# Kernel optimization log

Hardware: AMD Instinct MI355X
Metric: run time of the kernel (lower is better)

The kernel has to match this reference:

```python
import jax, jax.numpy as jnp
import numpy as np

B, A, F = 8192, 8, 256      # batch, n_agents, per-agent obs feature dim
NA = 16                     # n_actions per agent
H1, H2 = 1024, 1024
OBS_D = A * F               # 2048 flattened obs dim
ACT_D = A * NA              # 128 joint action dim
IN_D = OBS_D + ACT_D        # 2176 MLP input dim


def setup_inputs() -> dict:
    key = jax.random.key(0)
    ks = jax.random.split(key, 8)
    s = 0.02
    return {
        "obs": jax.random.normal(ks[0], (B, A, F), dtype=jnp.float32),
        "all_actions": jax.random.uniform(ks[1], (B, ACT_D), dtype=jnp.float32),
        # per-agent stacked MLP params (agent axis first)
        "W1": jax.random.normal(ks[2], (A, IN_D, H1), dtype=jnp.float32) * s,
        "b1": jnp.zeros((A, H1), dtype=jnp.float32),
        "W2": jax.random.normal(ks[3], (A, H1, H2), dtype=jnp.float32) * s,
        "b2": jnp.zeros((A, H2), dtype=jnp.float32),
        "W3": jax.random.normal(ks[4], (A, H2, NA), dtype=jnp.float32) * s,
        "b3": jnp.zeros((A, NA), dtype=jnp.float32),
    }


def reference(obs, all_actions, W1, b1, W2, b2, W3, b3):
    b_s = obs.shape[0]
    obs_flat = obs.reshape(b_s, OBS_D)                      # [B, A*F]
    # mask[a, g] = 0 on agent a's own action block, 1 elsewhere
    mask = 1.0 - jnp.repeat(jnp.eye(A, dtype=obs.dtype), NA, axis=1)  # [A, A*NA]
    # split W1 into obs / action columns (equivalent to concat-then-dense)
    W1o = W1[:, :OBS_D, :]                                  # [A, OBS_D, H1]
    W1a = W1[:, OBS_D:, :]                                  # [A, ACT_D, H1]
    h1 = jax.nn.relu(
        jnp.einsum("bd,adh->bah", obs_flat, W1o)
        + jnp.einsum("bg,ag,agh->bah", all_actions, mask, W1a)
        + b1
    )                                                        # [B, A, H1]
    h2 = jax.nn.relu(jnp.einsum("bah,ahk->bak", h1, W2) + b2)  # [B, A, H2]
    out = jnp.einsum("bak,akn->ban", h2, W3) + b3              # [B, A, NA]
    return out.reshape(b_s, A * NA)
```

## Files before the change

kernel.cpp:

```cpp
#include <hip/hip_runtime.h>
#include <hip/hip_bf16.h>
#include <cstdint>
#include <cstddef>

typedef __bf16 bf16;
typedef __attribute__((ext_vector_type(8))) __bf16 bf16x8;
typedef __attribute__((ext_vector_type(4))) float f32x4;
typedef __attribute__((ext_vector_type(4))) int i32x4;
typedef __attribute__((address_space(3))) const bf16* lds_cp;

#define B_SZ  8192
#define NAGENT 8
#define NA_N  16
#define OBS_DD 2048
#define ACT_DD 128
#define IN_DD 2176
#define H1_D  1024
#define H2_D  1024

#define BM 256
#define BN 256
#define BK 64
#define GRID_M (B_SZ / BM)
#define GRID_N (1024 / BN)

__device__ __forceinline__ void gload16(const void* g, void* l) {
    __builtin_amdgcn_global_load_lds(
        (__attribute__((address_space(1))) void*)(g),
        (__attribute__((address_space(3))) void*)(l), 16, 0, 0);
}

__global__ void k_prep(const float* __restrict__ obs, const float* __restrict__ act,
                       bf16* __restrict__ xb, const float* __restrict__ b3,
                       float* __restrict__ out, const float* __restrict__ W3,
                       bf16* __restrict__ w3t) {
    const int NX = B_SZ * (IN_DD / 8);
    const int NO = B_SZ * 128 / 4;
    const int NW3 = NAGENT * NA_N * H2_D;
    int idx = blockIdx.x * blockDim.x + threadIdx.x;
    if (idx < NX) {
        const int chunks = IN_DD / 8;
        int b = idx / chunks;
        int c8 = idx - b * chunks;
        const float* src = (c8 < OBS_DD / 8)
            ? (obs + (size_t)b * OBS_DD + c8 * 8)
            : (act + (size_t)b * ACT_DD + (c8 - OBS_DD / 8) * 8);
        float4 v0 = ((const float4*)src)[0];
        float4 v1 = ((const float4*)src)[1];
        bf16x8 o;
        o[0] = (bf16)v0.x; o[1] = (bf16)v0.y; o[2] = (bf16)v0.z; o[3] = (bf16)v0.w;
        o[4] = (bf16)v1.x; o[5] = (bf16)v1.y; o[6] = (bf16)v1.z; o[7] = (bf16)v1.w;
        ((bf16x8*)(xb + (size_t)b * IN_DD))[c8] = o;
    } else if (idx < NX + NO) {
        int i = idx - NX;
        int c = (i & 31) * 4;
        float4 v = make_float4(b3[c], b3[c + 1], b3[c + 2], b3[c + 3]);
        ((float4*)out)[i] = v;
    } else if (idx < NX + NO + NW3) {
        int i = idx - NX - NO;
        int a = i / (NA_N * H2_D);
        int n = (i / H2_D) % NA_N;
        int k = i % H2_D;
        w3t[i] = (bf16)W3[(size_t)a * H2_D * NA_N + (size_t)k * NA_N + n];
    }
}

__global__ void k_transpose_w12(const float* __restrict__ W1, bf16* __restrict__ W1T,
                                const float* __restrict__ W2, bf16* __restrict__ W2T) {
    __shared__ float tile[32][33];
    const int z = blockIdx.z;
    const bool isW1 = (z < 8);
    const int a = isW1 ? z : z - 8;
    const int K = isW1 ? IN_DD : H1_D;
    const int H = 1024;
    const int maskStart = isW1 ? OBS_DD : (1 << 30);
    if (!isW1 && blockIdx.x >= (H1_D / 32)) return;
    const float* s = (isW1 ? W1 : W2) + (size_t)a * K * H;
    bf16* d = (isW1 ? W1T : W2T) + (size_t)a * K * H;
    int k0 = blockIdx.x * 32, h0 = blockIdx.y * 32;
    int tx = threadIdx.x, ty = threadIdx.y;
    #pragma unroll
    for (int i = 0; i < 32; i += 8) {
        int k = k0 + ty + i;
        float v = s[(size_t)k * H + h0 + tx];
        if (k >= maskStart) {
            int g = k - maskStart;
            if ((g >> 4) == a) v = 0.f;
        }
        tile[ty + i][tx] = v;
    }
    __syncthreads();
    #pragma unroll
    for (int i = 0; i < 32; i += 8) {
        d[(size_t)(h0 + ty + i) * K + k0 + tx] = (bf16)tile[tx][ty + i];
    }
}

#define DSR4(d0, d1, d2, d3, addr, O0, O1, O2, O3)                      \
    asm volatile("ds_read_b128 %0, %4 offset:" #O0 "\n\t"               \
                 "ds_read_b128 %1, %4 offset:" #O1 "\n\t"               \
                 "ds_read_b128 %2, %4 offset:" #O2 "\n\t"               \
                 "ds_read_b128 %3, %4 offset:" #O3                      \
                 : "=&v"(d0), "=&v"(d1), "=&v"(d2), "=&v"(d3)           \
                 : "v"(addr))
#define DSR2(d0, d1, addr, O0, O1)                                      \
    asm volatile("ds_read_b128 %0, %2 offset:" #O0 "\n\t"               \
                 "ds_read_b128 %1, %2 offset:" #O1                      \
                 : "=&v"(d0), "=&v"(d1) : "v"(addr))

#define BC(x) __builtin_bit_cast(bf16x8, x)

template<int FUSE>
__global__ __launch_bounds__(512, 1)
void k_gemm256(const bf16* __restrict__ Ain, size_t aStride, int lda,
               const bf16* __restrict__ Bw, const float* __restrict__ bias,
               bf16* __restrict__ Cout, size_t cStride, int K,
               int aOff, int gridZ,
               const bf16* __restrict__ W3Tp, float* __restrict__ outp) {
    extern __shared__ bf16 lds[];

    const int tid = threadIdx.x;
    const int w = tid >> 6;
    const int l = tid & 63;

    int flat = blockIdx.x + GRID_M * (blockIdx.y + GRID_N * blockIdx.z);
    int q8 = (GRID_M * GRID_N * gridZ) >> 3;
    int lin2 = (flat & 7) * q8 + (flat >> 3);
    const int ntile = lin2 % GRID_N;
    int rest = lin2 / GRID_N;
    const int mt = rest % GRID_M;
    const int az = rest / GRID_M;
    const int aw = az + aOff;

    const int rowBase = mt * BM;
    const int colBase = ntile * BN;
    const bf16* Aag = Ain + (size_t)az * aStride;
    const bf16* Bag = Bw + (size_t)aw * (size_t)1024 * K;

    const int wr = (w >> 2) * 128;
    const int wc = (w & 3) * 64;
    const int lr = l & 15;
    const int lq = l >> 4;

    const int rowA = (wr + lr) * BK;
    const int rowB = (wc + lr) * BK;
    const int ck0 = ((lq ^ (lr & 7)) * 8);
    const int ck1 = (((4 + lq) ^ (lr & 7)) * 8);

    const int sRow = w * 16 + (l >> 3);
    const int sCol = ((l & 7) ^ (l >> 3)) * 8;
    const bf16* pA0 = Aag + (size_t)(rowBase + sRow) * lda + sCol;
    const bf16* pA1 = Aag + (size_t)(rowBase + 128 + sRow) * lda + sCol;
    const bf16* pB0 = Bag + (size_t)(colBase + sRow) * K + sCol;
    const bf16* pB1 = Bag + (size_t)(colBase + 128 + sRow) * K + sCol;
    const size_t l8a = (size_t)8 * lda;
    const size_t l8b = (size_t)8 * K;

    const int nkt = K / BK;

#define STAGE_A(t1, half) do {                                              \
        const bf16* g_ = ((half) ? pA1 : pA0) + (t1) * BK;                  \
        bf16* d_ = &lds[(((t1) & 1) * 16384) + (half) * 8192 + w * 1024];   \
        gload16(g_, d_);                                                    \
        gload16(g_ + l8a, d_ + 512);                                        \
    } while (0)
#define STAGE_B(t2, half) do {                                              \
        const bf16* g_ = ((half) ? pB1 : pB0) + (t2) * BK;                  \
        bf16* d_ = &lds[32768 + (((t2) & 1) * 16384) + (half) * 8192 + w * 1024]; \
        gload16(g_, d_);                                                    \
        gload16(g_ + l8b, d_ + 512);                                        \
    } while (0)

    f32x4 acc[8][4] = {};
    i32x4 rb0, rb1, rb2, rb3, rb4, rb5, rb6, rb7;
    i32x4 a0, a1, a2, a3, a4, a5, a6, a7, z0, z1;

#define CL8(M0, A0r, A1r, Bx0, Bx1, Bx2, Bx3)                               \
    do {                                                                    \
        acc[M0+0][0] = __builtin_amdgcn_mfma_f32_16x16x32_bf16(BC(A0r), BC(Bx0), acc[M0+0][0], 0, 0, 0); \
        acc[M0+1][0] = __builtin_amdgcn_mfma_f32_16x16x32_bf16(BC(A1r), BC(Bx0), acc[M0+1][0], 0, 0, 0); \
        acc[M0+0][1] = __builtin_amdgcn_mfma_f32_16x16x32_bf16(BC(A0r), BC(Bx1), acc[M0+0][1], 0, 0, 0); \
        acc[M0+1][1] = __builtin_amdgcn_mfma_f32_16x16x32_bf16(BC(A1r), BC(Bx1), acc[M0+1][1], 0, 0, 0); \
        acc[M0+0][2] = __builtin_amdgcn_mfma_f32_16x16x32_bf16(BC(A0r), BC(Bx2), acc[M0+0][2], 0, 0, 0); \
        acc[M0+1][2] = __builtin_amdgcn_mfma_f32_16x16x32_bf16(BC(A1r), BC(Bx2), acc[M0+1][2], 0, 0, 0); \
        acc[M0+0][3] = __builtin_amdgcn_mfma_f32_16x16x32_bf16(BC(A0r), BC(Bx3), acc[M0+0][3], 0, 0, 0); \
        acc[M0+1][3] = __builtin_amdgcn_mfma_f32_16x16x32_bf16(BC(A1r), BC(Bx3), acc[M0+1][3], 0, 0, 0); \
    } while (0)

#define WAITL(N)                                                            \
    asm volatile("s_waitcnt lgkmcnt(" #N ")" ::: "memory");                 \
    __builtin_amdgcn_sched_barrier(0)

    STAGE_A(0, 0); STAGE_A(0, 1);
    STAGE_B(0, 0); STAGE_B(0, 1);
    asm volatile("s_waitcnt vmcnt(0)" ::: "memory");
    __builtin_amdgcn_s_barrier();

    for (int t = 0; t < nkt; ++t) {
        const int dbuf = (t & 1) * 16384;
        lds_cp adrA0 = (lds_cp)lds + (dbuf + rowA + ck0);
        lds_cp adrA1 = (lds_cp)lds + (dbuf + rowA + ck1);
        lds_cp adrB0 = (lds_cp)lds + (32768 + dbuf + rowB + ck0);
        lds_cp adrB1 = (lds_cp)lds + (32768 + dbuf + rowB + ck1);

        DSR2(a0, a1, adrA0, 0, 2048);
        DSR4(rb0, rb1, rb2, rb3, adrB0, 0, 2048, 4096, 6144);
        DSR2(a2, a3, adrA0, 4096, 6144);

        WAITL(2);
        __builtin_amdgcn_s_setprio(1);
        CL8(0, a0, a1, rb0, rb1, rb2, rb3);
        __builtin_amdgcn_s_setprio(0);

        DSR2(a4, a5, adrA0, 8192, 10240);
        WAITL(2);
        __builtin_amdgcn_s_setprio(1);
        CL8(2, a2, a3, rb0, rb1, rb2, rb3);
        __builtin_amdgcn_s_setprio(0);

        DSR2(a6, a7, adrA0, 12288, 14336);
        if (t + 1 < nkt) {
            STAGE_A(t + 1, 0); STAGE_A(t + 1, 1);
            STAGE_B(t + 1, 0); STAGE_B(t + 1, 1);
        }
        WAITL(2);
        __builtin_amdgcn_s_setprio(1);
        CL8(4, a4, a5, rb0, rb1, rb2, rb3);
        __builtin_amdgcn_s_setprio(0);

        DSR2(z0, z1, adrA1, 0, 2048);
        DSR4(rb4, rb5, rb6, rb7, adrB1, 0, 2048, 4096, 6144);
        WAITL(6);
        __builtin_amdgcn_s_setprio(1);
        CL8(6, a6, a7, rb0, rb1, rb2, rb3);
        __builtin_amdgcn_s_setprio(0);

        DSR2(a0, a1, adrA1, 4096, 6144);
        WAITL(2);
        __builtin_amdgcn_s_setprio(1);
        CL8(0, z0, z1, rb4, rb5, rb6, rb7);
        __builtin_amdgcn_s_setprio(0);

        DSR2(a2, a3, adrA1, 8192, 10240);
        WAITL(2);
        __builtin_amdgcn_s_setprio(1);
        CL8(2, a0, a1, rb4, rb5, rb6, rb7);
        __builtin_amdgcn_s_setprio(0);

        DSR2(a4, a5, adrA1, 12288, 14336);
        WAITL(2);
        __builtin_amdgcn_s_setprio(1);
        CL8(4, a2, a3, rb4, rb5, rb6, rb7);
        __builtin_amdgcn_s_setprio(0);

        asm volatile("s_waitcnt vmcnt(0)" ::: "memory");
        WAITL(0);
        __builtin_amdgcn_s_setprio(1);
        CL8(6, a4, a5, rb4, rb5, rb6, rb7);
        __builtin_amdgcn_s_setprio(0);

        __builtin_amdgcn_s_barrier();
    }
#undef STAGE_A
#undef STAGE_B
#undef CL8
#undef WAITL

    __syncthreads();
    const float* bAg = bias + (size_t)aw * 1024;
    float bb4[4];
    #pragma unroll
    for (int n = 0; n < 4; ++n) bb4[n] = bAg[colBase + wc + n * 16 + lr];
    #pragma unroll
    for (int m = 0; m < 8; ++m)
        #pragma unroll
        for (int n = 0; n < 4; ++n)
            #pragma unroll
            for (int r = 0; r < 4; ++r) {
                float v = acc[m][n][r] + bb4[n];
                v = fmaxf(v, 0.f);
                int row = wr + m * 16 + lq * 4 + r;
                int col = wc + n * 16 + lr;
                lds[row * 256 + ((((col >> 3) ^ (row & 7)) << 3) | (col & 7))] = (bf16)v;
            }
    __syncthreads();

    if constexpr (!FUSE) {
        bf16* Cg = Cout + (size_t)az * cStride + (size_t)rowBase * 1024 + colBase;
        const int er = tid >> 5;
        const int ec = tid & 31;
        #pragma unroll
        for (int i = 0; i < 16; ++i) {
            int row = i * 16 + er;
            int phys = ec ^ (row & 7);
            *(bf16x8*)&Cg[(size_t)row * 1024 + ec * 8] =
                *(const bf16x8*)&lds[row * 256 + phys * 8];
        }
    } else {
        const bf16* w3a = W3Tp + (size_t)aw * NA_N * H2_D;
        f32x4 oacc[2] = {};
        const int frow0 = w * 32;
        #pragma unroll
        for (int ks = 0; ks < 8; ++ks) {
            bf16x8 bfrag = *(const bf16x8*)&w3a[(size_t)lr * H2_D + colBase + ks * 32 + lq * 8];
            #pragma unroll
            for (int mm = 0; mm < 2; ++mm) {
                int row = frow0 + mm * 16 + lr;
                int lc = (ks * 4 + lq) ^ (row & 7);
                bf16x8 afrag = *(const bf16x8*)&lds[row * 256 + lc * 8];
                oacc[mm] = __builtin_amdgcn_mfma_f32_16x16x32_bf16(afrag, bfrag, oacc[mm], 0, 0, 0);
            }
        }
        #pragma unroll
        for (int mm = 0; mm < 2; ++mm)
            #pragma unroll
            for (int r = 0; r < 4; ++r)
                atomicAdd(&outp[(size_t)(rowBase + frow0 + mm * 16 + lq * 4 + r) * 128
                                + aw * NA_N + lr], oacc[mm][r]);
    }
}

extern "C" void kernel_launch(void* const* d_in, const int* in_sizes, int n_in,
                              void* d_out, int out_size, void* d_ws, size_t ws_size,
                              hipStream_t stream) {
    const float* obs = (const float*)d_in[0];
    const float* act = (const float*)d_in[1];
    const float* W1 = (const float*)d_in[2];
    const float* b1 = (const float*)d_in[3];
    const float* W2 = (const float*)d_in[4];
    const float* b2 = (const float*)d_in[5];
    const float* W3 = (const float*)d_in[6];
    const float* b3 = (const float*)d_in[7];
    float* out = (float*)d_out;

    const size_t SZ_XB  = (size_t)B_SZ * IN_DD * 2;
    const size_t SZ_W1T = (size_t)NAGENT * H1_D * IN_DD * 2;
    const size_t SZ_W2T = (size_t)NAGENT * H1_D * H2_D * 2;
    const size_t SZ_W3T = (size_t)NAGENT * NA_N * H2_D * 2;
    const size_t SZ_H1  = (size_t)B_SZ * H1_D * 2;
    const size_t SZ_FIX = SZ_XB + SZ_W1T + SZ_W2T + SZ_W3T;

    char* ws = (char*)d_ws;
    bf16* Xb  = (bf16*)ws;
    bf16* W1T = (bf16*)(ws + SZ_XB);
    bf16* W2T = (bf16*)(ws + SZ_XB + SZ_W1T);
    bf16* W3T = (bf16*)(ws + SZ_XB + SZ_W1T + SZ_W2T);
    char* hbase = ws + SZ_FIX;

    int G = 8;
    while (G > 1 && ws_size < SZ_FIX + (size_t)G * SZ_H1) G >>= 1;

    (void)hipFuncSetAttribute((const void*)k_gemm256<0>,
                              hipFuncAttributeMaxDynamicSharedMemorySize, 131072);
    (void)hipFuncSetAttribute((const void*)k_gemm256<1>,
                              hipFuncAttributeMaxDynamicSharedMemorySize, 131072);

    {
        const int NX = B_SZ * (IN_DD / 8);
        const int NO = B_SZ * 128 / 4;
        const int NW3 = NAGENT * NA_N * H2_D;
        int n = NX + NO + NW3;
        k_prep<<<(n + 255) / 256, 256, 0, stream>>>(obs, act, Xb, b3, out, W3, W3T);
    }
    k_transpose_w12<<<dim3(IN_DD / 32, 1024 / 32, 16), dim3(32, 8), 0, stream>>>(
        W1, W1T, W2, W2T);

    const size_t agElems = (size_t)B_SZ * H1_D;
    bf16* h1 = (bf16*)hbase;

    for (int g0 = 0; g0 < NAGENT; g0 += G) {
        k_gemm256<0><<<dim3(GRID_M, GRID_N, G), 512, 131072, stream>>>(
            Xb, 0, IN_DD, W1T, b1, h1, agElems, IN_DD, g0, G, nullptr, nullptr);
        k_gemm256<1><<<dim3(GRID_M, GRID_N, G), 512, 131072, stream>>>(
            h1, agElems, H1_D, W2T, b2, nullptr, 0, H1_D, g0, G, W3T, out);
    }
    (void)in_sizes; (void)n_in; (void)out_size;
}
```

Before: 407.1 us.

## Switch main GEMM to 32x32x16 MFMA with new LDS swizzle and read schedule

Replaces the 16x16x32 bf16 MFMA tiling in the 256x256 GEMM with 32x32x16 MFMA instructions, using 4x2 accumulators of 16 floats per wave instead of 8x4 of 4. The LDS staging swizzle gains an extra XOR term, and the fragment reads are reorganised into four k-slices with ping-pong register sets. The aim is fewer LDS fragment reads per FLOP and higher MFMA throughput per instruction. The epilogue row/column mapping is rewritten for the 32x32 output layout. This risks bank conflicts and a swizzle mismatch with the store pattern, and the prefetch now issues earlier in the iteration.

```diff
diff --git a/kernel.cpp b/kernel.cpp
--- a/kernel.cpp
+++ b/kernel.cpp
@@ -6,6 +6,7 @@
 typedef __bf16 bf16;
 typedef __attribute__((ext_vector_type(8))) __bf16 bf16x8;
 typedef __attribute__((ext_vector_type(4))) float f32x4;
+typedef __attribute__((ext_vector_type(16))) float f32x16;
 typedef __attribute__((ext_vector_type(4))) int i32x4;
 typedef __attribute__((address_space(3))) const bf16* lds_cp;
 
@@ -29,6 +30,9 @@
         (__attribute__((address_space(1))) void*)(g),
         (__attribute__((address_space(3))) void*)(l), 16, 0, 0);
 }
+
+#define MFMA32(a, b, c) __builtin_amdgcn_mfma_f32_32x32x16_bf16((a), (b), (c), 0, 0, 0)
+#define BC(x) __builtin_bit_cast(bf16x8, x)
 
 __global__ void k_prep(const float* __restrict__ obs, const float* __restrict__ act,
                        bf16* __restrict__ xb, const float* __restrict__ b3,
@@ -108,8 +112,6 @@
                  "ds_read_b128 %1, %2 offset:" #O1                      \
                  : "=&v"(d0), "=&v"(d1) : "v"(addr))
 
-#define BC(x) __builtin_bit_cast(bf16x8, x)
-
 template<int FUSE>
 __global__ __launch_bounds__(512, 1)
 void k_gemm256(const bf16* __restrict__ Ain, size_t aStride, int lda,
@@ -139,16 +141,22 @@
 
     const int wr = (w >> 2) * 128;
     const int wc = (w & 3) * 64;
+    const int r31 = l & 31;
+    const int hi = l >> 5;
+    const int x7 = l & 7;
+    const int hb = (l >> 4) & 1;
     const int lr = l & 15;
     const int lq = l >> 4;
 
-    const int rowA = (wr + lr) * BK;
-    const int rowB = (wc + lr) * BK;
-    const int ck0 = ((lq ^ (lr & 7)) * 8);
-    const int ck1 = (((4 + lq) ^ (lr & 7)) * 8);
+    const int arow = (wr + r31) * BK;
+    const int brow = (wc + r31) * BK;
+    const int cs0 = ((0 + hi) ^ x7 ^ (hb << 2)) * 8;
+    const int cs1 = ((2 + hi) ^ x7 ^ (hb << 2)) * 8;
+    const int cs2 = ((4 + hi) ^ x7 ^ (hb << 2)) * 8;
+    const int cs3 = ((6 + hi) ^ x7 ^ (hb << 2)) * 8;
 
     const int sRow = w * 16 + (l >> 3);
-    const int sCol = ((l & 7) ^ (l >> 3)) * 8;
+    const int sCol = ((l & 7) ^ (l >> 3) ^ ((w & 1) << 2)) * 8;
     const bf16* pA0 = Aag + (size_t)(rowBase + sRow) * lda + sCol;
     const bf16* pA1 = Aag + (size_t)(rowBase + 128 + sRow) * lda + sCol;
     const bf16* pB0 = Bag + (size_t)(colBase + sRow) * K + sCol;
@@ -171,20 +179,20 @@
         gload16(g_ + l8b, d_ + 512);                                        \
     } while (0)
 
-    f32x4 acc[8][4] = {};
-    i32x4 rb0, rb1, rb2, rb3, rb4, rb5, rb6, rb7;
-    i32x4 a0, a1, a2, a3, a4, a5, a6, a7, z0, z1;
-
-#define CL8(M0, A0r, A1r, Bx0, Bx1, Bx2, Bx3)                               \
+    f32x16 acc[4][2] = {};
+    i32x4 fa0, fa1, fa2, fa3, fb0, fb1;
+    i32x4 ga0, ga1, ga2, ga3, gb0, gb1;
+
+#define CLK(A0r, A1r, A2r, A3r, B0r, B1r)                                   \
     do {                                                                    \
-        acc[M0+0][0] = __builtin_amdgcn_mfma_f32_16x16x32_bf16(BC(A0r), BC(Bx0), acc[M0+0][0], 0, 0, 0); \
-        acc[M0+1][0] = __builtin_amdgcn_mfma_f32_16x16x32_bf16(BC(A1r), BC(Bx0), acc[M0+1][0], 0, 0, 0); \
-        acc[M0+0][1] = __builtin_amdgcn_mfma_f32_16x16x32_bf16(BC(A0r), BC(Bx1), acc[M0+0][1], 0, 0, 0); \
-        acc[M0+1][1] = __builtin_amdgcn_mfma_f32_16x16x32_bf16(BC(A1r), BC(Bx1), acc[M0+1][1], 0, 0, 0); \
-        acc[M0+0][2] = __builtin_amdgcn_mfma_f32_16x16x32_bf16(BC(A0r), BC(Bx2), acc[M0+0][2], 0, 0, 0); \
-        acc[M0+1][2] = __builtin_amdgcn_mfma_f32_16x16x32_bf16(BC(A1r), BC(Bx2), acc[M0+1][2], 0, 0, 0); \
-        acc[M0+0][3] = __builtin_amdgcn_mfma_f32_16x16x32_bf16(BC(A0r), BC(Bx3), acc[M0+0][3], 0, 0, 0); \
-        acc[M0+1][3] = __builtin_amdgcn_mfma_f32_16x16x32_bf16(BC(A1r), BC(Bx3), acc[M0+1][3], 0, 0, 0); \
+        acc[0][0] = MFMA32(BC(A0r), BC(B0r), acc[0][0]);                    \
+        acc[1][0] = MFMA32(BC(A1r), BC(B0r), acc[1][0]);                    \
+        acc[0][1] = MFMA32(BC(A0r), BC(B1r), acc[0][1]);                    \
+        acc[1][1] = MFMA32(BC(A1r), BC(B1r), acc[1][1]);                    \
+        acc[2][0] = MFMA32(BC(A2r), BC(B0r), acc[2][0]);                    \
+        acc[3][0] = MFMA32(BC(A3r), BC(B0r), acc[3][0]);                    \
+        acc[2][1] = MFMA32(BC(A2r), BC(B1r), acc[2][1]);                    \
+        acc[3][1] = MFMA32(BC(A3r), BC(B1r), acc[3][1]);                    \
     } while (0)
 
 #define WAITL(N)                                                            \
@@ -198,89 +206,72 @@
 
     for (int t = 0; t < nkt; ++t) {
         const int dbuf = (t & 1) * 16384;
-        lds_cp adrA0 = (lds_cp)lds + (dbuf + rowA + ck0);
-        lds_cp adrA1 = (lds_cp)lds + (dbuf + rowA + ck1);
-        lds_cp adrB0 = (lds_cp)lds + (32768 + dbuf + rowB + ck0);
-        lds_cp adrB1 = (lds_cp)lds + (32768 + dbuf + rowB + ck1);
-
-        DSR2(a0, a1, adrA0, 0, 2048);
-        DSR4(rb0, rb1, rb2, rb3, adrB0, 0, 2048, 4096, 6144);
-        DSR2(a2, a3, adrA0, 4096, 6144);
-
-        WAITL(2);
-        __builtin_amdgcn_s_setprio(1);
-        CL8(0, a0, a1, rb0, rb1, rb2, rb3);
-        __builtin_amdgcn_s_setprio(0);
-
-        DSR2(a4, a5, adrA0, 8192, 10240);
-        WAITL(2);
-        __builtin_amdgcn_s_setprio(1);
-        CL8(2, a2, a3, rb0, rb1, rb2, rb3);
-        __builtin_amdgcn_s_setprio(0);
-
-        DSR2(a6, a7, adrA0, 12288, 14336);
+        lds_cp aA0 = (lds_cp)lds + (dbuf + arow + cs0);
+        lds_cp aA1 = (lds_cp)lds + (dbuf + arow + cs1);
+        lds_cp aA2 = (lds_cp)lds + (dbuf + arow + cs2);
+        lds_cp aA3 = (lds_cp)lds + (dbuf + arow + cs3);
+        lds_cp aB0 = (lds_cp)lds + (32768 + dbuf + brow + cs0);
+        lds_cp aB1 = (lds_cp)lds + (32768 + dbuf + brow + cs1);
+        lds_cp aB2 = (lds_cp)lds + (32768 + dbuf + brow + cs2);
+        lds_cp aB3 = (lds_cp)lds + (32768 + dbuf + brow + cs3);
+
+        DSR4(fa0, fa1, fa2, fa3, aA0, 0, 4096, 8192, 12288);
+        DSR2(fb0, fb1, aB0, 0, 4096);
+        DSR4(ga0, ga1, ga2, ga3, aA1, 0, 4096, 8192, 12288);
+        DSR2(gb0, gb1, aB1, 0, 4096);
+
         if (t + 1 < nkt) {
             STAGE_A(t + 1, 0); STAGE_A(t + 1, 1);
             STAGE_B(t + 1, 0); STAGE_B(t + 1, 1);
         }
-        WAITL(2);
-        __builtin_amdgcn_s_setprio(1);
-        CL8(4, a4, a5, rb0, rb1, rb2, rb3);
-        __builtin_amdgcn_s_setprio(0);
-
-        DSR2(z0, z1, adrA1, 0, 2048);
-        DSR4(rb4, rb5, rb6, rb7, adrB1, 0, 2048, 4096, 6144);
+
         WAITL(6);
         __builtin_amdgcn_s_setprio(1);
-        CL8(6, a6, a7, rb0, rb1, rb2, rb3);
+        CLK(fa0, fa1, fa2, fa3, fb0, fb1);
         __builtin_amdgcn_s_setprio(0);
 
-        DSR2(a0, a1, adrA1, 4096, 6144);
-        WAITL(2);
+        DSR4(fa0, fa1, fa2, fa3, aA2, 0, 4096, 8192, 12288);
+        DSR2(fb0, fb1, aB2, 0, 4096);
+        WAITL(6);
         __builtin_amdgcn_s_setprio(1);
-        CL8(0, z0, z1, rb4, rb5, rb6, rb7);
+        CLK(ga0, ga1, ga2, ga3, gb0, gb1);
         __builtin_amdgcn_s_setprio(0);
 
-        DSR2(a2, a3, adrA1, 8192, 10240);
-        WAITL(2);
+        DSR4(ga0, ga1, ga2, ga3, aA3, 0, 4096, 8192, 12288);
+        DSR2(gb0, gb1, aB3, 0, 4096);
+        WAITL(6);
         __builtin_amdgcn_s_setprio(1);
-        CL8(2, a0, a1, rb4, rb5, rb6, rb7);
-        __builtin_amdgcn_s_setprio(0);
-
-        DSR2(a4, a5, adrA1, 12288, 14336);
-        WAITL(2);
-        __builtin_amdgcn_s_setprio(1);
-        CL8(4, a2, a3, rb4, rb5, rb6, rb7);
+        CLK(fa0, fa1, fa2, fa3, fb0, fb1);
         __builtin_amdgcn_s_setprio(0);
 
         asm volatile("s_waitcnt vmcnt(0)" ::: "memory");
         WAITL(0);
         __builtin_amdgcn_s_setprio(1);
-        CL8(6, a4, a5, rb4, rb5, rb6, rb7);
+        CLK(ga0, ga1, ga2, ga3, gb0, gb1);
         __builtin_amdgcn_s_setprio(0);
 
         __builtin_amdgcn_s_barrier();
     }
 #undef STAGE_A
 #undef STAGE_B
-#undef CL8
+#undef CLK
 #undef WAITL
 
     __syncthreads();
     const float* bAg = bias + (size_t)aw * 1024;
-    float bb4[4];
+    float bb2[2];
     #pragma unroll
-    for (int n = 0; n < 4; ++n) bb4[n] = bAg[colBase + wc + n * 16 + lr];
+    for (int n = 0; n < 2; ++n) bb2[n] = bAg[colBase + wc + n * 32 + r31];
     #pragma unroll
-    for (int m = 0; m < 8; ++m)
+    for (int m = 0; m < 4; ++m)
         #pragma unroll
-        for (int n = 0; n < 4; ++n)
+        for (int n = 0; n < 2; ++n)
             #pragma unroll
-            for (int r = 0; r < 4; ++r) {
-                float v = acc[m][n][r] + bb4[n];
+            for (int r = 0; r < 16; ++r) {
+                float v = acc[m][n][r] + bb2[n];
                 v = fmaxf(v, 0.f);
-                int row = wr + m * 16 + lq * 4 + r;
-                int col = wc + n * 16 + lr;
+                int row = wr + m * 32 + (r & 3) + 8 * (r >> 2) + 4 * hi;
+                int col = wc + n * 32 + r31;
                 lds[row * 256 + ((((col >> 3) ^ (row & 7)) << 3) | (col & 7))] = (bf16)v;
             }
     __syncthreads();
```

Measured after the change: 495.9 us. 1.22x slower.
